# Kernel tuning notes

Measured on AMD Instinct MI355X. Metric: run time of the kernel, lower is better.

Reference implementation:

```python
import jax, jax.numpy as jnp
import numpy as np

N, S, E, H = 2, 2048, 1024, 16
D = E // H  # head dim = 64


def setup_inputs() -> dict:
    key = jax.random.key(0)
    ks = jax.random.split(key, 9)
    queries = jax.random.normal(ks[0], (N, S, E), dtype=jnp.float32)
    keys = jax.random.normal(ks[1], (N, S, E), dtype=jnp.float32)
    values = jax.random.normal(ks[2], (N, S, E), dtype=jnp.float32)
    mask = jax.random.randint(ks[3], (N, H, S, S), 0, 2, dtype=jnp.int32)
    # torch nn.Linear weights: shape (out_features, in_features), y = x @ W.T
    sc = 1.0 / np.sqrt(E)
    Wq = jax.random.uniform(ks[4], (E, E), jnp.float32, -sc, sc)
    Wk = jax.random.uniform(ks[5], (E, E), jnp.float32, -sc, sc)
    Wv = jax.random.uniform(ks[6], (E, E), jnp.float32, -sc, sc)
    Wo = jax.random.uniform(ks[7], (E, E), jnp.float32, -sc, sc)
    bo = jax.random.uniform(ks[8], (E,), jnp.float32, -sc, sc)
    return {"queries": queries, "keys": keys, "values": values, "mask": mask,
            "Wq": Wq, "Wk": Wk, "Wv": Wv, "Wo": Wo, "bo": bo}


def reference(queries, keys, values, mask, Wq, Wk, Wv, Wo, bo):
    n, d_q, _ = queries.shape
    d_k = keys.shape[1]
    q = (queries @ Wq.T).reshape(n, d_q, H, D)
    k = (keys @ Wk.T).reshape(n, d_k, H, D)
    v = (values @ Wv.T).reshape(n, d_k, H, D)
    energy = jnp.einsum('nqhd,nkhd->nhqk', q, k)
    energy = jnp.where(mask == 0, jnp.float32(-1e20), energy)
    # NOTE: module scales by sqrt of KEY SEQUENCE LENGTH, not head dim
    attn = jax.nn.softmax(energy / (d_k ** 0.5), axis=3)
    out = jnp.einsum('nhql,nlhd->nqhd', attn, v).reshape(n, d_q, E)
    return out @ Wo.T + bo
```

## Files before the change

### kernel.cpp

```cpp
#include <hip/hip_runtime.h>
#include <hip/hip_bf16.h>

#define DEVI __device__ __forceinline__

typedef __bf16 bf16x8 __attribute__((ext_vector_type(8)));
typedef float f32x4 __attribute__((ext_vector_type(4)));
typedef unsigned short u16x8 __attribute__((ext_vector_type(8)));
typedef unsigned short u16x4 __attribute__((ext_vector_type(4)));

constexpr int Nn = 2, Ss = 2048, Ee = 1024, Hh = 16;
constexpr int Ms = Nn * Ss;
constexpr float SCALE = 0.022097086912079608f;

constexpr size_t SZ_X   = (size_t)Ms * Ee;
constexpr size_t OFF_QB = 0;
constexpr size_t OFF_KB = SZ_X;
constexpr size_t OFF_VB = 2 * SZ_X;
constexpr size_t OFF_XQ = 3 * SZ_X;
constexpr size_t OFF_W  = 6 * SZ_X;
constexpr size_t OFF_ATTN = OFF_XQ;

DEVI unsigned short f2bf(float f) {
  unsigned int u = __builtin_bit_cast(unsigned int, f);
  u += 0x7fffu + ((u >> 16) & 1u);
  return (unsigned short)(u >> 16);
}

DEVI void async16(const void* g, void* l) {
  __builtin_amdgcn_global_load_lds(
      (const __attribute__((address_space(1))) void*)g,
      (__attribute__((address_space(3))) void*)l, 16, 0, 0);
}

DEVI f32x4 mfma_bf16(bf16x8 a, bf16x8 b, f32x4 c) {
  return __builtin_amdgcn_mfma_f32_16x16x32_bf16(a, b, c, 0, 0, 0);
}

__global__ __launch_bounds__(256) void cvt_batch(
    const float* __restrict__ s0, const float* __restrict__ s1,
    const float* __restrict__ s2, const float* __restrict__ s3,
    unsigned short* __restrict__ dbase, size_t dstride, int n4)
{
  const float* s = (blockIdx.z == 0) ? s0 : (blockIdx.z == 1) ? s1
                 : (blockIdx.z == 2) ? s2 : s3;
  unsigned short* d = dbase + (size_t)blockIdx.z * dstride;
  const int i = blockIdx.x * 256 + threadIdx.x;
  if (i >= n4) return;
  const float4 v = reinterpret_cast<const float4*>(s)[i];
  u16x4 o = { f2bf(v.x), f2bf(v.y), f2bf(v.z), f2bf(v.w) };
  reinterpret_cast<u16x4*>(d)[i] = o;
}

template <bool WRITE_F32>
__global__ __launch_bounds__(256) void gemm_bt(
    const unsigned short* __restrict__ Abase,
    const unsigned short* __restrict__ Bbase,
    unsigned short* __restrict__ Cbase,
    float* __restrict__ Cf,
    const float* __restrict__ bias,
    size_t strideA, size_t strideB, size_t strideC)
{
  constexpr int N = 1024, K = 1024;
  __shared__ unsigned short As[128 * 32];
  __shared__ unsigned short Bs[128 * 32];

  const int z = blockIdx.z;
  const unsigned short* A = Abase + (size_t)z * strideA;
  const unsigned short* B = Bbase + (size_t)z * strideB;

  const int tid = threadIdx.x;
  const int lane = tid & 63, w = tid >> 6;
  const int lr = lane & 15, lg = lane >> 4;
  const int m0 = blockIdx.y * 128, n0 = blockIdx.x * 128;
  const int wr = (w >> 1) * 64, wc = (w & 1) * 64;

  const f32x4 zero = {0.f, 0.f, 0.f, 0.f};
  f32x4 acc[4][4];
  for (int a = 0; a < 4; ++a)
    for (int b = 0; b < 4; ++b) acc[a][b] = zero;

  for (int k0 = 0; k0 < K; k0 += 32) {
#pragma unroll
    for (int ii = 0; ii < 2; ++ii) {
      const int i = 2 * w + ii;
      const int boff = i * 1024 + lane * 16;
      const int row = boff >> 6;
      const int colb = boff & 63;
      const char* ga = (const char*)A + ((size_t)(m0 + row) * K + k0) * 2 + colb;
      const char* gb = (const char*)B + ((size_t)(n0 + row) * K + k0) * 2 + colb;
      async16(ga, (char*)As + i * 1024);
      async16(gb, (char*)Bs + i * 1024);
    }
    __syncthreads();

    bf16x8 aF[4], bF[4];
#pragma unroll
    for (int rb = 0; rb < 4; ++rb)
      aF[rb] = *(const bf16x8*)(As + (wr + rb * 16 + lr) * 32 + lg * 8);
#pragma unroll
    for (int cb = 0; cb < 4; ++cb)
      bF[cb] = *(const bf16x8*)(Bs + (wc + cb * 16 + lr) * 32 + lg * 8);
#pragma unroll
    for (int rb = 0; rb < 4; ++rb)
#pragma unroll
      for (int cb = 0; cb < 4; ++cb)
        acc[rb][cb] = mfma_bf16(aF[rb], bF[cb], acc[rb][cb]);
    __syncthreads();
  }

#pragma unroll
  for (int rb = 0; rb < 4; ++rb) {
#pragma unroll
    for (int cb = 0; cb < 4; ++cb) {
#pragma unroll
      for (int j = 0; j < 4; ++j) {
        const int row = m0 + wr + rb * 16 + lg * 4 + j;
        const int col = n0 + wc + cb * 16 + lr;
        const float v = acc[rb][cb][j];
        if constexpr (WRITE_F32) {
          Cf[(size_t)row * N + col] = v + bias[col];
        } else {
          unsigned short* C = Cbase + (size_t)z * strideC;
          C[(size_t)row * N + col] = f2bf(v);
        }
      }
    }
  }
}

__global__ __launch_bounds__(256) void attn_kernel(
    const unsigned short* __restrict__ Qb,
    const unsigned short* __restrict__ Kb,
    const unsigned short* __restrict__ Vb,
    const int* __restrict__ mask,
    unsigned short* __restrict__ Ob)
{
  __shared__ unsigned short Kl[64 * 72];
  __shared__ unsigned short Vt[64 * 72];
  __shared__ unsigned short Pl[64 * 72];

  const int tid = threadIdx.x;
  const int lane = tid & 63, w = tid >> 6;
  const int lr = lane & 15, lg = lane >> 4;
  const int n = blockIdx.y >> 4, h = blockIdx.y & 15;
  const int q0 = blockIdx.x * 64;

  bf16x8 aQ[2];
  {
    const unsigned short* qp =
        Qb + ((size_t)(n * Ss + q0 + w * 16 + lr)) * Ee + h * 64 + lg * 8;
    aQ[0] = *(const bf16x8*)(qp);
    aQ[1] = *(const bf16x8*)(qp + 32);
  }

  const f32x4 zero = {0.f, 0.f, 0.f, 0.f};
  f32x4 oacc[4] = {zero, zero, zero, zero};
  float rs[4] = {0.f, 0.f, 0.f, 0.f};

  const int rr = tid >> 3, ch = tid & 7;
  const size_t mbase = ((size_t)(n * Hh + h)) * Ss * Ss;

  for (int kt = 0; kt < Ss / 64; ++kt) {
    const int k0 = kt * 64;
#pragma unroll
    for (int ps = 0; ps < 2; ++ps) {
      const int row = rr + ps * 32;
      const size_t gb = ((size_t)(n * Ss + k0 + row)) * Ee + h * 64 + ch * 8;
      u16x8 kv = *(const u16x8*)(Kb + gb);
      *(u16x8*)(Kl + row * 72 + ch * 8) = kv;
      u16x8 vv = *(const u16x8*)(Vb + gb);
#pragma unroll
      for (int j = 0; j < 8; ++j) Vt[(ch * 8 + j) * 72 + row] = vv[j];
    }
    __syncthreads();

    int mv[4][4];
#pragma unroll
    for (int cb = 0; cb < 4; ++cb)
#pragma unroll
      for (int j = 0; j < 4; ++j) {
        const int qr = w * 16 + lg * 4 + j;
        const int kk = cb * 16 + lr;
        mv[cb][j] = mask[mbase + (size_t)(q0 + qr) * Ss + k0 + kk];
      }

    f32x4 s4[4];
#pragma unroll
    for (int cb = 0; cb < 4; ++cb) {
      f32x4 a = zero;
#pragma unroll
      for (int kc = 0; kc < 2; ++kc) {
        bf16x8 bF = *(const bf16x8*)(Kl + (cb * 16 + lr) * 72 + kc * 32 + lg * 8);
        a = mfma_bf16(aQ[kc], bF, a);
      }
      s4[cb] = a;
    }

#pragma unroll
    for (int cb = 0; cb < 4; ++cb)
#pragma unroll
      for (int j = 0; j < 4; ++j) {
        const int qr = w * 16 + lg * 4 + j;
        const int kk = cb * 16 + lr;
        float p = mv[cb][j] ? __expf(s4[cb][j] * SCALE) : 0.f;
        rs[j] += p;
        Pl[qr * 72 + kk] = f2bf(p);
      }

    bf16x8 aP[2];
    aP[0] = *(const bf16x8*)(Pl + (w * 16 + lr) * 72 + lg * 8);
    aP[1] = *(const bf16x8*)(Pl + (w * 16 + lr) * 72 + 32 + lg * 8);
#pragma unroll
    for (int db = 0; db < 4; ++db)
#pragma unroll
      for (int kc = 0; kc < 2; ++kc) {
        bf16x8 bV = *(const bf16x8*)(Vt + (db * 16 + lr) * 72 + kc * 32 + lg * 8);
        oacc[db] = mfma_bf16(aP[kc], bV, oacc[db]);
      }
    __syncthreads();
  }

#pragma unroll
  for (int j = 0; j < 4; ++j) {
    float r = rs[j];
#pragma unroll
    for (int m = 1; m < 16; m <<= 1) r += __shfl_xor(r, m, 64);
    rs[j] = 1.0f / r;
  }
#pragma unroll
  for (int db = 0; db < 4; ++db)
#pragma unroll
    for (int j = 0; j < 4; ++j) {
      const int qr = q0 + w * 16 + lg * 4 + j;
      Ob[((size_t)(n * Ss + qr)) * Ee + h * 64 + db * 16 + lr] =
          f2bf(oacc[db][j] * rs[j]);
    }
}

extern "C" void kernel_launch(void* const* d_in, const int* in_sizes, int n_in,
                              void* d_out, int out_size, void* d_ws, size_t ws_size,
                              hipStream_t stream) {
  const float* qin = (const float*)d_in[0];
  const float* kin = (const float*)d_in[1];
  const float* vin = (const float*)d_in[2];
  const int*   msk = (const int*)d_in[3];
  const float* Wq  = (const float*)d_in[4];
  const float* Wk  = (const float*)d_in[5];
  const float* Wv  = (const float*)d_in[6];
  const float* Wo  = (const float*)d_in[7];
  const float* bo  = (const float*)d_in[8];
  unsigned short* ws = (unsigned short*)d_ws;

  cvt_batch<<<dim3((unsigned)(SZ_X / 4 / 256), 1, 3), 256, 0, stream>>>(
      qin, kin, vin, nullptr, ws + OFF_XQ, SZ_X, (int)(SZ_X / 4));
  cvt_batch<<<dim3((unsigned)((size_t)Ee * Ee / 4 / 256), 1, 4), 256, 0, stream>>>(
      Wq, Wk, Wv, Wo, ws + OFF_W, (size_t)Ee * Ee, (int)((size_t)Ee * Ee / 4));

  gemm_bt<false><<<dim3(8, 32, 3), 256, 0, stream>>>(
      ws + OFF_XQ, ws + OFF_W, ws + OFF_QB, nullptr, nullptr,
      SZ_X, (size_t)Ee * Ee, SZ_X);

  attn_kernel<<<dim3(32, 32), 256, 0, stream>>>(
      ws + OFF_QB, ws + OFF_KB, ws + OFF_VB, msk, ws + OFF_ATTN);

  gemm_bt<true><<<dim3(8, 32, 1), 256, 0, stream>>>(
      ws + OFF_ATTN, ws + OFF_W + 3 * (size_t)Ee * Ee, nullptr,
      (float*)d_out, bo, 0, 0, 0);
}
```

Measured before the change: 252.2 us.

## Double-buffer K/V tiles with async LDS loads and pre-transposed V projection

The V projection is now computed as Wv·Xᵀ, so V is written already transposed (head-dim major). The attention kernel can then stream K and Vᵀ tiles into XOR-swizzled, double-buffered LDS with global_load_lds instead of doing a scalar transpose scatter each iteration. Mask values for the next tile are prefetched with nontemporal loads, and the MFMA sections run at raised wave priority. This targets the load latency and LDS transpose/bank-conflict costs in the attention loop, in exchange for more LDS use and a separate GEMM launch for V.

```diff
diff --git a/kernel.cpp b/kernel.cpp
--- a/kernel.cpp
+++ b/kernel.cpp
@@ -58,9 +58,9 @@
     unsigned short* __restrict__ Cbase,
     float* __restrict__ Cf,
     const float* __restrict__ bias,
-    size_t strideA, size_t strideB, size_t strideC)
+    size_t strideA, size_t strideB, size_t strideC, int ldC)
 {
-  constexpr int N = 1024, K = 1024;
+  constexpr int K = 1024;
   __shared__ unsigned short As[128 * 32];
   __shared__ unsigned short Bs[128 * 32];
 
@@ -118,10 +118,10 @@
         const int col = n0 + wc + cb * 16 + lr;
         const float v = acc[rb][cb][j];
         if constexpr (WRITE_F32) {
-          Cf[(size_t)row * N + col] = v + bias[col];
+          Cf[(size_t)row * ldC + col] = v + bias[col];
         } else {
           unsigned short* C = Cbase + (size_t)z * strideC;
-          C[(size_t)row * N + col] = f2bf(v);
+          C[(size_t)row * ldC + col] = f2bf(v);
         }
       }
     }
@@ -131,12 +131,12 @@
 __global__ __launch_bounds__(256) void attn_kernel(
     const unsigned short* __restrict__ Qb,
     const unsigned short* __restrict__ Kb,
-    const unsigned short* __restrict__ Vb,
+    const unsigned short* __restrict__ Vtb,
     const int* __restrict__ mask,
     unsigned short* __restrict__ Ob)
 {
-  __shared__ unsigned short Kl[64 * 72];
-  __shared__ unsigned short Vt[64 * 72];
+  __shared__ unsigned short Kl0[64 * 64], Kl1[64 * 64];
+  __shared__ unsigned short Vl0[64 * 64], Vl1[64 * 64];
   __shared__ unsigned short Pl[64 * 72];
 
   const int tid = threadIdx.x;
@@ -153,48 +153,77 @@
     aQ[1] = *(const bf16x8*)(qp + 32);
   }
 
+  const int sig0 = (w * 2) * 64 + lane;
+  const int row0 = sig0 >> 3;
+  const int c0 = (sig0 & 7) ^ (row0 & 7);
+  const int row1 = row0 + 8;
+  const int c1 = (sig0 & 7) ^ (row1 & 7);
+  const int ldsb0 = (w * 2 + 0) * 1024;
+  const int ldsb1 = (w * 2 + 1) * 1024;
+
+  const unsigned short* kp0 = Kb + ((size_t)(n * Ss + row0) * Ee + h * 64 + c0 * 8);
+  const unsigned short* kp1 = Kb + ((size_t)(n * Ss + row1) * Ee + h * 64 + c1 * 8);
+  const unsigned short* vp0 = Vtb + ((size_t)(h * 64 + row0) * Ms + n * Ss + c0 * 8);
+  const unsigned short* vp1 = Vtb + ((size_t)(h * 64 + row1) * Ms + n * Ss + c1 * 8);
+
+  const int* mp = mask + ((size_t)(n * Hh + h)) * Ss * Ss
+                       + (size_t)(q0 + w * 16 + lg * 4) * Ss + lr;
+
   const f32x4 zero = {0.f, 0.f, 0.f, 0.f};
   f32x4 oacc[4] = {zero, zero, zero, zero};
   float rs[4] = {0.f, 0.f, 0.f, 0.f};
 
-  const int rr = tid >> 3, ch = tid & 7;
-  const size_t mbase = ((size_t)(n * Hh + h)) * Ss * Ss;
-
+  async16(kp0, (char*)Kl0 + ldsb0);
+  async16(kp1, (char*)Kl0 + ldsb1);
+  async16(vp0, (char*)Vl0 + ldsb0);
+  async16(vp1, (char*)Vl0 + ldsb1);
+  kp0 += (size_t)64 * Ee; kp1 += (size_t)64 * Ee; vp0 += 64; vp1 += 64;
+
+  int mv[4][4], mvN[4][4];
+#pragma unroll
+  for (int cb = 0; cb < 4; ++cb)
+#pragma unroll
+    for (int j = 0; j < 4; ++j)
+      mv[cb][j] = __builtin_nontemporal_load(mp + (size_t)j * Ss + cb * 16);
+
+  __syncthreads();
+
+  int cur = 0;
   for (int kt = 0; kt < Ss / 64; ++kt) {
-    const int k0 = kt * 64;
-#pragma unroll
-    for (int ps = 0; ps < 2; ++ps) {
-      const int row = rr + ps * 32;
-      const size_t gb = ((size_t)(n * Ss + k0 + row)) * Ee + h * 64 + ch * 8;
-      u16x8 kv = *(const u16x8*)(Kb + gb);
-      *(u16x8*)(Kl + row * 72 + ch * 8) = kv;
-      u16x8 vv = *(const u16x8*)(Vb + gb);
-#pragma unroll
-      for (int j = 0; j < 8; ++j) Vt[(ch * 8 + j) * 72 + row] = vv[j];
-    }
-    __syncthreads();
-
-    int mv[4][4];
-#pragma unroll
-    for (int cb = 0; cb < 4; ++cb)
-#pragma unroll
-      for (int j = 0; j < 4; ++j) {
-        const int qr = w * 16 + lg * 4 + j;
-        const int kk = cb * 16 + lr;
-        mv[cb][j] = mask[mbase + (size_t)(q0 + qr) * Ss + k0 + kk];
-      }
+    const unsigned short* Kc = cur ? Kl1 : Kl0;
+    const unsigned short* Vc = cur ? Vl1 : Vl0;
+    unsigned short* Kn = cur ? Kl0 : Kl1;
+    unsigned short* Vn = cur ? Vl0 : Vl1;
+
+    if (kt + 1 < Ss / 64) {
+      async16(kp0, (char*)Kn + ldsb0);
+      async16(kp1, (char*)Kn + ldsb1);
+      async16(vp0, (char*)Vn + ldsb0);
+      async16(vp1, (char*)Vn + ldsb1);
+      kp0 += (size_t)64 * Ee; kp1 += (size_t)64 * Ee; vp0 += 64; vp1 += 64;
+#pragma unroll
+      for (int cb = 0; cb < 4; ++cb)
+#pragma unroll
+        for (int j = 0; j < 4; ++j)
+          mvN[cb][j] = __builtin_nontemporal_load(
+              mp + (size_t)(kt + 1) * 64 + (size_t)j * Ss + cb * 16);
+    }
 
     f32x4 s4[4];
+    __builtin_amdgcn_s_setprio(1);
 #pragma unroll
     for (int cb = 0; cb < 4; ++cb) {
       f32x4 a = zero;
 #pragma unroll
       for (int kc = 0; kc < 2; ++kc) {
-        bf16x8 bF = *(const bf16x8*)(Kl + (cb * 16 + lr) * 72 + kc * 32 + lg * 8);
+        const int row = cb * 16 + lr;
+        bf16x8 bF = *(const bf16x8*)((const char*)Kc + row * 128 +
+                                     (((kc * 4 + lg) ^ (row & 7)) * 16));
         a = mfma_bf16(aQ[kc], bF, a);
       }
       s4[cb] = a;
     }
+    __builtin_amdgcn_s_setprio(0);
 
 #pragma unroll
     for (int cb = 0; cb < 4; ++cb)
@@ -210,14 +239,24 @@
     bf16x8 aP[2];
     aP[0] = *(const bf16x8*)(Pl + (w * 16 + lr) * 72 + lg * 8);
     aP[1] = *(const bf16x8*)(Pl + (w * 16 + lr) * 72 + 32 + lg * 8);
+    __builtin_amdgcn_s_setprio(1);
 #pragma unroll
     for (int db = 0; db < 4; ++db)
 #pragma unroll
       for (int kc = 0; kc < 2; ++kc) {
-        bf16x8 bV = *(const bf16x8*)(Vt + (db * 16 + lr) * 72 + kc * 32 + lg * 8);
+        const int row = db * 16 + lr;
+        bf16x8 bV = *(const bf16x8*)((const char*)Vc + row * 128 +
+                                     (((kc * 4 + lg) ^ (row & 7)) * 16));
         oacc[db] = mfma_bf16(aP[kc], bV, oacc[db]);
       }
+    __builtin_amdgcn_s_setprio(0);
+
     __syncthreads();
+#pragma unroll
+    for (int cb = 0; cb < 4; ++cb)
+#pragma unroll
+      for (int j = 0; j < 4; ++j) mv[cb][j] = mvN[cb][j];
+    cur ^= 1;
   }
 
 #pragma unroll
@@ -250,20 +289,25 @@
   const float* Wo  = (const float*)d_in[7];
   const float* bo  = (const float*)d_in[8];
   unsigned short* ws = (unsigned short*)d_ws;
+  const size_t EE = (size_t)Ee * Ee;
 
   cvt_batch<<<dim3((unsigned)(SZ_X / 4 / 256), 1, 3), 256, 0, stream>>>(
       qin, kin, vin, nullptr, ws + OFF_XQ, SZ_X, (int)(SZ_X / 4));
-  cvt_batch<<<dim3((unsigned)((size_t)Ee * Ee / 4 / 256), 1, 4), 256, 0, stream>>>(
-      Wq, Wk, Wv, Wo, ws + OFF_W, (size_t)Ee * Ee, (int)((size_t)Ee * Ee / 4));
-
-  gemm_bt<false><<<dim3(8, 32, 3), 256, 0, stream>>>(
+  cvt_batch<<<dim3((unsigned)(EE / 4 / 256), 1, 4), 256, 0, stream>>>(
+      Wq, Wk, Wv, Wo, ws + OFF_W, EE, (int)(EE / 4));
+
+  gemm_bt<false><<<dim3(8, 32, 2), 256, 0, stream>>>(
       ws + OFF_XQ, ws + OFF_W, ws + OFF_QB, nullptr, nullptr,
-      SZ_X, (size_t)Ee * Ee, SZ_X);
+      SZ_X, EE, SZ_X, Ee);
+
+  gemm_bt<false><<<dim3(32, 8, 1), 256, 0, stream>>>(
+      ws + OFF_W + 2 * EE, ws + OFF_XQ + 2 * SZ_X, ws + OFF_VB, nullptr, nullptr,
+      0, 0, 0, Ms);
 
   attn_kernel<<<dim3(32, 32), 256, 0, stream>>>(
       ws + OFF_QB, ws + OFF_KB, ws + OFF_VB, msk, ws + OFF_ATTN);
 
   gemm_bt<true><<<dim3(8, 32, 1), 256, 0, stream>>>(
-      ws + OFF_ATTN, ws + OFF_W + 3 * (size_t)Ee * Ee, nullptr,
-      (float*)d_out, bo, 0, 0, 0);
-}
+      ws + OFF_ATTN, ws + OFF_W + 3 * EE, nullptr,
+      (float*)d_out, bo, 0, 0, 0, Ee);
+}
```

New measurement: 250.7 us. Within noise of the previous version (-0.6%).
